# Kernel tuning notes

Hardware: AMD Instinct MI355X
Metric: run time of the kernel (lower is better)

Reference implementation:

```python
import jax, jax.numpy as jnp
import numpy as np

ALPHA = 0.2  # LeakyReLU negative slope
NEG = -9e15


def setup_inputs() -> dict:
    key = jax.random.key(0)
    k1, k2, k3, k4 = jax.random.split(key, 4)
    N, F_in, F_out = 8192, 512, 64
    h = jax.random.normal(k1, (N, F_in), dtype=jnp.float32)
    adj = jax.random.randint(k2, (N, N), 0, 2, dtype=jnp.int32)
    # xavier_uniform with gain=1.414
    def xavier(k, shape, gain=1.414):
        fan_in, fan_out = shape[0], shape[1]
        bound = gain * np.sqrt(6.0 / (fan_in + fan_out))
        return jax.random.uniform(k, shape, jnp.float32, -bound, bound)
    W = xavier(k3, (F_in, F_out))
    a = xavier(k4, (2 * F_out, 1))
    return {"h": h, "adj": adj, "W": W, "a": a}


def reference(h, adj, W, a):
    F_out = W.shape[1]
    Wh = h @ W                                   # [N, F_out]
    # e_ij = LeakyReLU([Wh_i || Wh_j] . a) = LeakyReLU(Wh.a1 + (Wh.a2)^T)
    e1 = Wh @ a[:F_out, 0]                       # [N]
    e2 = Wh @ a[F_out:, 0]                       # [N]
    e = jax.nn.leaky_relu(e1[:, None] + e2[None, :], ALPHA)  # [N, N]
    e = jnp.where(adj > 0, e, NEG)
    attention = jax.nn.softmax(e, axis=1)        # dropout p=0.0 -> identity
    h_prime = attention @ Wh                     # [N, F_out]
    return jax.nn.elu(h_prime)                   # concat=True
```

## Files before the change

### kernel.cpp

```cpp
#include <hip/hip_runtime.h>
#include <hip/hip_bf16.h>
#include <stdint.h>

typedef __attribute__((ext_vector_type(8))) short short8;
typedef __attribute__((ext_vector_type(4))) float f32x4;

#define NSLICE 8
#define SLICE_J 1024
#define CHUNKS 16
#define L2E 1.44269504f

static __device__ __forceinline__ short f2bf(float f) {
    unsigned int u = __float_as_uint(f);
    u += 0x7fffu + ((u >> 16) & 1u);
    return (short)(u >> 16);
}

static __device__ __forceinline__ short welem(int a, float e2s, float e1s, float& lsum) {
    float x = e1s + e2s;
    x = fmaxf(x, 0.f) + 0.2f * fminf(x, 0.f);
    float w = __builtin_amdgcn_exp2f(x);
    w = (a > 0) ? w : 0.f;
    lsum += w;
    return f2bf(w);
}

__global__ __launch_bounds__(256)
void gat_wh(const float* __restrict__ h, const float* __restrict__ W,
            const float* __restrict__ a, short* __restrict__ whT,
            float* __restrict__ e1, float* __restrict__ e2)
{
    const int lane = threadIdx.x & 63;
    const int wave = threadIdx.x >> 6;
    const int row0 = blockIdx.x * 16 + wave * 4;

    float acc[4] = {0.f, 0.f, 0.f, 0.f};
#pragma unroll 8
    for (int c = 0; c < 512; ++c) {
        const float wv = W[c * 64 + lane];
#pragma unroll
        for (int r = 0; r < 4; ++r)
            acc[r] += h[(size_t)(row0 + r) * 512 + c] * wv;
    }

    const float a1v = a[lane];
    const float a2v = a[64 + lane];
    const int f    = lane >> 4;
    const int r16n = lane & 15;
#pragma unroll
    for (int r = 0; r < 4; ++r) {
        float p1 = acc[r] * a1v;
        float p2 = acc[r] * a2v;
#pragma unroll
        for (int off = 32; off; off >>= 1) {
            p1 += __shfl_xor(p1, off);
            p2 += __shfl_xor(p2, off);
        }
        if (lane == 0) { e1[row0 + r] = p1; e2[row0 + r] = p2; }
        const int j = row0 + r;
        const int kin = j & 63;
        const int frag = (kin >> 5) & 1, qk = (kin >> 3) & 3, t = kin & 7;
        whT[(size_t)(j >> 6) * 4096 + (f * 2 + frag) * 512 + qk * 128 + r16n * 8 + t]
            = f2bf(acc[r]);
    }
}

__global__ __launch_bounds__(256)
void gat_attn(const int* __restrict__ adj, const short* __restrict__ whT,
              const float* __restrict__ e1, const float* __restrict__ e2,
              float* __restrict__ lpart, float* __restrict__ opart)
{
    __shared__ float se2[SLICE_J];
    const int bid = blockIdx.x;
    const int s   = bid & (NSLICE - 1);
    const int rb  = bid >> 3;
    const int tid = threadIdx.x;

    {
        float4 v = *reinterpret_cast<const float4*>(e2 + s * SLICE_J + tid * 4);
        v.x *= L2E; v.y *= L2E; v.z *= L2E; v.w *= L2E;
        *reinterpret_cast<float4*>(se2 + tid * 4) = v;
    }
    __syncthreads();

    const int lane = tid & 63;
    const int wave = tid >> 6;
    const int quad = lane >> 4;
    const int r16  = lane & 15;
    const int rowBase = rb * 64 + wave * 16;
    const int row  = rowBase + r16;
    const float e1s = e1[row] * L2E;
    const size_t adjRow = (size_t)row * 8192 + (size_t)s * SLICE_J;

    float lsum = 0.f;
    f32x4 acc[4];
#pragma unroll
    for (int ff = 0; ff < 4; ++ff) acc[ff] = (f32x4){0.f, 0.f, 0.f, 0.f};

    for (int ch = 0; ch < CHUNKS; ++ch) {
        const int j0 = ch * 64 + quad * 8;
        const int4 A0 = *reinterpret_cast<const int4*>(adj + adjRow + j0);
        const int4 A1 = *reinterpret_cast<const int4*>(adj + adjRow + j0 + 4);
        const int4 A2 = *reinterpret_cast<const int4*>(adj + adjRow + j0 + 32);
        const int4 A3 = *reinterpret_cast<const int4*>(adj + adjRow + j0 + 36);
        const float4 E0 = *reinterpret_cast<const float4*>(se2 + j0);
        const float4 E1 = *reinterpret_cast<const float4*>(se2 + j0 + 4);
        const float4 E2 = *reinterpret_cast<const float4*>(se2 + j0 + 32);
        const float4 E3 = *reinterpret_cast<const float4*>(se2 + j0 + 36);

        short8 af0, af1;
        af0[0] = welem(A0.x, E0.x, e1s, lsum);
        af0[1] = welem(A0.y, E0.y, e1s, lsum);
        af0[2] = welem(A0.z, E0.z, e1s, lsum);
        af0[3] = welem(A0.w, E0.w, e1s, lsum);
        af0[4] = welem(A1.x, E1.x, e1s, lsum);
        af0[5] = welem(A1.y, E1.y, e1s, lsum);
        af0[6] = welem(A1.z, E1.z, e1s, lsum);
        af0[7] = welem(A1.w, E1.w, e1s, lsum);
        af1[0] = welem(A2.x, E2.x, e1s, lsum);
        af1[1] = welem(A2.y, E2.y, e1s, lsum);
        af1[2] = welem(A2.z, E2.z, e1s, lsum);
        af1[3] = welem(A2.w, E2.w, e1s, lsum);
        af1[4] = welem(A3.x, E3.x, e1s, lsum);
        af1[5] = welem(A3.y, E3.y, e1s, lsum);
        af1[6] = welem(A3.z, E3.z, e1s, lsum);
        af1[7] = welem(A3.w, E3.w, e1s, lsum);

        const short* wtile = whT + (size_t)(s * 16 + ch) * 4096 + lane * 8;
#pragma unroll
        for (int ff = 0; ff < 4; ++ff) {
            const short8 b0 = *reinterpret_cast<const short8*>(wtile + (ff * 2 + 0) * 512);
            const short8 b1 = *reinterpret_cast<const short8*>(wtile + (ff * 2 + 1) * 512);
            acc[ff] = __builtin_amdgcn_mfma_f32_16x16x32_bf16(af0, b0, acc[ff], 0, 0, 0);
            acc[ff] = __builtin_amdgcn_mfma_f32_16x16x32_bf16(af1, b1, acc[ff], 0, 0, 0);
        }
    }

    lsum += __shfl_xor(lsum, 16);
    lsum += __shfl_xor(lsum, 32);
    if (lane < 16) lpart[s * 8192 + rowBase + lane] = lsum;

#pragma unroll
    for (int ff = 0; ff < 4; ++ff) {
#pragma unroll
        for (int rg = 0; rg < 4; ++rg) {
            const int orow = rowBase + quad * 4 + rg;
            const int ocol = ff * 16 + r16;
            opart[((size_t)s * 8192 + orow) * 64 + ocol] = acc[ff][rg];
        }
    }
}

__global__ __launch_bounds__(256)
void gat_combine(const float* __restrict__ lpart, const float* __restrict__ opart,
                 float* __restrict__ out)
{
    const int gid = blockIdx.x * 256 + threadIdx.x;
    const int row = gid >> 6;
    const int f   = gid & 63;

    float lsum = 0.f, osum = 0.f;
#pragma unroll
    for (int s = 0; s < NSLICE; ++s) {
        lsum += lpart[s * 8192 + row];
        osum += opart[((size_t)s * 8192 + row) * 64 + f];
    }
    const float v = osum / lsum;
    out[gid] = (v > 0.f) ? v : (__expf(v) - 1.f);
}

extern "C" void kernel_launch(void* const* d_in, const int* in_sizes, int n_in,
                              void* d_out, int out_size, void* d_ws, size_t ws_size,
                              hipStream_t stream) {
    const float* h   = (const float*)d_in[0];
    const int*   adj = (const int*)d_in[1];
    const float* W   = (const float*)d_in[2];
    const float* a   = (const float*)d_in[3];
    float* out = (float*)d_out;

    char* ws = (char*)d_ws;
    short* whT   = (short*)ws;
    float* e1    = (float*)(ws + (1u << 20));
    float* e2    = (float*)(ws + (1u << 20) + (32u << 10));
    float* lpart = (float*)(ws + (1u << 20) + (64u << 10));
    float* opart = (float*)(ws + (2u << 20));

    gat_wh<<<512, 256, 0, stream>>>(h, W, a, whT, e1, e2);
    gat_attn<<<128 * NSLICE, 256, 0, stream>>>(adj, whT, e1, e2, lpart, opart);
    gat_combine<<<out_size / 256, 256, 0, stream>>>(lpart, opart, out);
}
```

Measured before the change: 433.9 us.

## Split-K the Wh projection, add pack kernel, prefetch adj and pack bf16 in attn

The projection h@W is split four ways along K across 2048 blocks writing fp32 partials, and a new pack kernel reduces them, computes e1/e2 and writes the bf16 swizzled layout. This is meant to fix the low parallelism of the old 512-block projection. In the attention kernel, adjacency loads for the next chunk are software-prefetched, and LeakyReLU becomes a single fma with abs. The bf16 conversion uses the packed v_cvt_pk_bf16_f32 instruction, the row sum is split into two accumulators, and launch bounds request 4 blocks per CU. The changes add an extra kernel launch plus an 8 MB partial buffer round trip, and raise register pressure from the prefetch.

New measurement: 467.8 us. 7.8% more time.

```diff
diff --git a/kernel.cpp b/kernel.cpp
--- a/kernel.cpp
+++ b/kernel.cpp
@@ -16,56 +16,74 @@
     return (short)(u >> 16);
 }
 
-static __device__ __forceinline__ short welem(int a, float e2s, float e1s, float& lsum) {
+static __device__ __forceinline__ float wfloat(int a, float e2s, float e1s, float& lsum) {
     float x = e1s + e2s;
-    x = fmaxf(x, 0.f) + 0.2f * fminf(x, 0.f);
+    x = fmaf(0.4f, fabsf(x), 0.6f * x);
     float w = __builtin_amdgcn_exp2f(x);
     w = (a > 0) ? w : 0.f;
     lsum += w;
-    return f2bf(w);
+    return w;
+}
+
+static __device__ __forceinline__ unsigned pkbf16(float lo, float hi) {
+    unsigned r;
+    asm("v_cvt_pk_bf16_f32 %0, %1, %2" : "=v"(r) : "v"(lo), "v"(hi));
+    return r;
 }
 
 __global__ __launch_bounds__(256)
-void gat_wh(const float* __restrict__ h, const float* __restrict__ W,
-            const float* __restrict__ a, short* __restrict__ whT,
-            float* __restrict__ e1, float* __restrict__ e2)
+void gat_wh_part(const float* __restrict__ h, const float* __restrict__ W,
+                 float* __restrict__ whp)
 {
     const int lane = threadIdx.x & 63;
     const int wave = threadIdx.x >> 6;
-    const int row0 = blockIdx.x * 16 + wave * 4;
+    const int ks   = blockIdx.x & 3;
+    const int row0 = (blockIdx.x >> 2) * 16 + wave * 4;
+    const int c0   = ks * 128;
 
     float acc[4] = {0.f, 0.f, 0.f, 0.f};
 #pragma unroll 8
-    for (int c = 0; c < 512; ++c) {
+    for (int ci = 0; ci < 128; ++ci) {
+        const int c = c0 + ci;
         const float wv = W[c * 64 + lane];
 #pragma unroll
         for (int r = 0; r < 4; ++r)
             acc[r] += h[(size_t)(row0 + r) * 512 + c] * wv;
     }
-
-    const float a1v = a[lane];
-    const float a2v = a[64 + lane];
-    const int f    = lane >> 4;
-    const int r16n = lane & 15;
-#pragma unroll
-    for (int r = 0; r < 4; ++r) {
-        float p1 = acc[r] * a1v;
-        float p2 = acc[r] * a2v;
-#pragma unroll
-        for (int off = 32; off; off >>= 1) {
-            p1 += __shfl_xor(p1, off);
-            p2 += __shfl_xor(p2, off);
-        }
-        if (lane == 0) { e1[row0 + r] = p1; e2[row0 + r] = p2; }
-        const int j = row0 + r;
-        const int kin = j & 63;
-        const int frag = (kin >> 5) & 1, qk = (kin >> 3) & 3, t = kin & 7;
-        whT[(size_t)(j >> 6) * 4096 + (f * 2 + frag) * 512 + qk * 128 + r16n * 8 + t]
-            = f2bf(acc[r]);
-    }
+#pragma unroll
+    for (int r = 0; r < 4; ++r)
+        whp[((size_t)ks << 19) + (size_t)(row0 + r) * 64 + lane] = acc[r];
 }
 
 __global__ __launch_bounds__(256)
+void gat_pack(const float* __restrict__ whp, const float* __restrict__ a,
+              short* __restrict__ whT, float* __restrict__ e1, float* __restrict__ e2)
+{
+    const int lane = threadIdx.x & 63;
+    const int wave = threadIdx.x >> 6;
+    const int row  = blockIdx.x * 4 + wave;
+
+    float acc = 0.f;
+#pragma unroll
+    for (int ks = 0; ks < 4; ++ks)
+        acc += whp[((size_t)ks << 19) + (size_t)row * 64 + lane];
+
+    float p1 = acc * a[lane];
+    float p2 = acc * a[64 + lane];
+#pragma unroll
+    for (int off = 32; off; off >>= 1) {
+        p1 += __shfl_xor(p1, off);
+        p2 += __shfl_xor(p2, off);
+    }
+    if (lane == 0) { e1[row] = p1; e2[row] = p2; }
+
+    const int kin = row & 63;
+    const int frag = (kin >> 5) & 1, qk = (kin >> 3) & 3, t = kin & 7;
+    whT[(size_t)(row >> 6) * 4096 + ((lane >> 4) * 2 + frag) * 512 + qk * 128
+        + (lane & 15) * 8 + t] = f2bf(acc);
+}
+
+__global__ __launch_bounds__(256, 4)
 void gat_attn(const int* __restrict__ adj, const short* __restrict__ whT,
               const float* __restrict__ e1, const float* __restrict__ e2,
               float* __restrict__ lpart, float* __restrict__ opart)
@@ -90,52 +108,75 @@
     const int rowBase = rb * 64 + wave * 16;
     const int row  = rowBase + r16;
     const float e1s = e1[row] * L2E;
-    const size_t adjRow = (size_t)row * 8192 + (size_t)s * SLICE_J;
-
-    float lsum = 0.f;
+    const int* __restrict__ arow = adj + (size_t)row * 8192 + s * SLICE_J + quad * 8;
+
+    float lsa = 0.f, lsb = 0.f;
     f32x4 acc[4];
 #pragma unroll
     for (int ff = 0; ff < 4; ++ff) acc[ff] = (f32x4){0.f, 0.f, 0.f, 0.f};
 
+    int4 A0 = *reinterpret_cast<const int4*>(arow + 0);
+    int4 A1 = *reinterpret_cast<const int4*>(arow + 4);
+    int4 A2 = *reinterpret_cast<const int4*>(arow + 32);
+    int4 A3 = *reinterpret_cast<const int4*>(arow + 36);
+
     for (int ch = 0; ch < CHUNKS; ++ch) {
+        const int jn = ((ch + 1) & (CHUNKS - 1)) * 64;
+        const int4 N0 = *reinterpret_cast<const int4*>(arow + jn + 0);
+        const int4 N1 = *reinterpret_cast<const int4*>(arow + jn + 4);
+        const int4 N2 = *reinterpret_cast<const int4*>(arow + jn + 32);
+        const int4 N3 = *reinterpret_cast<const int4*>(arow + jn + 36);
+
         const int j0 = ch * 64 + quad * 8;
-        const int4 A0 = *reinterpret_cast<const int4*>(adj + adjRow + j0);
-        const int4 A1 = *reinterpret_cast<const int4*>(adj + adjRow + j0 + 4);
-        const int4 A2 = *reinterpret_cast<const int4*>(adj + adjRow + j0 + 32);
-        const int4 A3 = *reinterpret_cast<const int4*>(adj + adjRow + j0 + 36);
         const float4 E0 = *reinterpret_cast<const float4*>(se2 + j0);
         const float4 E1 = *reinterpret_cast<const float4*>(se2 + j0 + 4);
         const float4 E2 = *reinterpret_cast<const float4*>(se2 + j0 + 32);
         const float4 E3 = *reinterpret_cast<const float4*>(se2 + j0 + 36);
 
-        short8 af0, af1;
-        af0[0] = welem(A0.x, E0.x, e1s, lsum);
-        af0[1] = welem(A0.y, E0.y, e1s, lsum);
-        af0[2] = welem(A0.z, E0.z, e1s, lsum);
-        af0[3] = welem(A0.w, E0.w, e1s, lsum);
-        af0[4] = welem(A1.x, E1.x, e1s, lsum);
-        af0[5] = welem(A1.y, E1.y, e1s, lsum);
-        af0[6] = welem(A1.z, E1.z, e1s, lsum);
-        af0[7] = welem(A1.w, E1.w, e1s, lsum);
-        af1[0] = welem(A2.x, E2.x, e1s, lsum);
-        af1[1] = welem(A2.y, E2.y, e1s, lsum);
-        af1[2] = welem(A2.z, E2.z, e1s, lsum);
-        af1[3] = welem(A2.w, E2.w, e1s, lsum);
-        af1[4] = welem(A3.x, E3.x, e1s, lsum);
-        af1[5] = welem(A3.y, E3.y, e1s, lsum);
-        af1[6] = welem(A3.z, E3.z, e1s, lsum);
-        af1[7] = welem(A3.w, E3.w, e1s, lsum);
+        union U { unsigned u[4]; short8 s8; };
+        U af0, af1;
+        {
+            const float w0 = wfloat(A0.x, E0.x, e1s, lsa);
+            const float w1 = wfloat(A0.y, E0.y, e1s, lsa);
+            const float w2 = wfloat(A0.z, E0.z, e1s, lsa);
+            const float w3 = wfloat(A0.w, E0.w, e1s, lsa);
+            const float w4 = wfloat(A1.x, E1.x, e1s, lsa);
+            const float w5 = wfloat(A1.y, E1.y, e1s, lsa);
+            const float w6 = wfloat(A1.z, E1.z, e1s, lsa);
+            const float w7 = wfloat(A1.w, E1.w, e1s, lsa);
+            af0.u[0] = pkbf16(w0, w1);
+            af0.u[1] = pkbf16(w2, w3);
+            af0.u[2] = pkbf16(w4, w5);
+            af0.u[3] = pkbf16(w6, w7);
+        }
+        {
+            const float w0 = wfloat(A2.x, E2.x, e1s, lsb);
+            const float w1 = wfloat(A2.y, E2.y, e1s, lsb);
+            const float w2 = wfloat(A2.z, E2.z, e1s, lsb);
+            const float w3 = wfloat(A2.w, E2.w, e1s, lsb);
+            const float w4 = wfloat(A3.x, E3.x, e1s, lsb);
+            const float w5 = wfloat(A3.y, E3.y, e1s, lsb);
+            const float w6 = wfloat(A3.z, E3.z, e1s, lsb);
+            const float w7 = wfloat(A3.w, E3.w, e1s, lsb);
+            af1.u[0] = pkbf16(w0, w1);
+            af1.u[1] = pkbf16(w2, w3);
+            af1.u[2] = pkbf16(w4, w5);
+            af1.u[3] = pkbf16(w6, w7);
+        }
 
         const short* wtile = whT + (size_t)(s * 16 + ch) * 4096 + lane * 8;
 #pragma unroll
         for (int ff = 0; ff < 4; ++ff) {
             const short8 b0 = *reinterpret_cast<const short8*>(wtile + (ff * 2 + 0) * 512);
             const short8 b1 = *reinterpret_cast<const short8*>(wtile + (ff * 2 + 1) * 512);
-            acc[ff] = __builtin_amdgcn_mfma_f32_16x16x32_bf16(af0, b0, acc[ff], 0, 0, 0);
-            acc[ff] = __builtin_amdgcn_mfma_f32_16x16x32_bf16(af1, b1, acc[ff], 0, 0, 0);
-        }
-    }
-
+            acc[ff] = __builtin_amdgcn_mfma_f32_16x16x32_bf16(af0.s8, b0, acc[ff], 0, 0, 0);
+            acc[ff] = __builtin_amdgcn_mfma_f32_16x16x32_bf16(af1.s8, b1, acc[ff], 0, 0, 0);
+        }
+
+        A0 = N0; A1 = N1; A2 = N2; A3 = N3;
+    }
+
+    float lsum = lsa + lsb;
     lsum += __shfl_xor(lsum, 16);
     lsum += __shfl_xor(lsum, 32);
     if (lane < 16) lpart[s * 8192 + rowBase + lane] = lsum;
@@ -184,8 +225,10 @@
     float* e2    = (float*)(ws + (1u << 20) + (32u << 10));
     float* lpart = (float*)(ws + (1u << 20) + (64u << 10));
     float* opart = (float*)(ws + (2u << 20));
-
-    gat_wh<<<512, 256, 0, stream>>>(h, W, a, whT, e1, e2);
+    float* whp   = (float*)(ws + (32u << 20));
+
+    gat_wh_part<<<2048, 256, 0, stream>>>(h, W, whp);
+    gat_pack<<<2048, 256, 0, stream>>>(whp, a, whT, e1, e2);
     gat_attn<<<128 * NSLICE, 256, 0, stream>>>(adj, whT, e1, e2, lpart, opart);
     gat_combine<<<out_size / 256, 256, 0, stream>>>(lpart, opart, out);
 }
```
